# Kernel optimization log

Hardware: AMD Instinct MI355X
Metric: run time of the kernel (lower is better)

Reference implementation:

```python
import jax, jax.numpy as jnp
import numpy as np

D, Z, A, H, E = 1024, 256, 32, 512, 1024  # deterministic, state, action, stochastic(hidden), embedding
MIN_STD = 0.1


def _linear_params(key, out_dim, in_dim, scale=0.02):
    kw, kb = jax.random.split(key)
    W = jax.random.normal(kw, (out_dim, in_dim), jnp.float32) * scale
    b = jax.random.normal(kb, (out_dim,), jnp.float32) * scale
    return W, b


def setup_inputs() -> dict:
    key = jax.random.key(0)
    ks = jax.random.split(key, 16)
    T, B = 64, 512
    inp = {
        "prev_state": jax.random.normal(ks[0], (B, Z), jnp.float32),
        "prev_belief": jax.random.normal(ks[1], (B, D), jnp.float32),
        "actions": jax.random.normal(ks[2], (T, B, A), jnp.float32),
        "observations": jax.random.normal(ks[3], (T, B, E), jnp.float32),
        "nonterminals": jnp.ones((T, B, 1), jnp.float32),
        "noise_belief": jax.random.normal(ks[4], (T, B, D), jnp.float32),
        "noise_prior": jax.random.normal(ks[5], (T, B, Z), jnp.float32),
        "noise_post": jax.random.normal(ks[6], (T, B, Z), jnp.float32),
    }
    inp["W_sa"], inp["b_sa"] = _linear_params(ks[7], D, Z + A)      # fc_embed_state_action
    inp["W_ih"], inp["b_ih"] = _linear_params(ks[8], 3 * D, D)       # GRUCell input weights
    inp["W_hh"], inp["b_hh"] = _linear_params(ks[9], 3 * D, D)       # GRUCell hidden weights
    inp["W_eb"], inp["b_eb"] = _linear_params(ks[10], H, D)          # fc_embed_belief
    inp["W_bq"], inp["b_bq"] = _linear_params(ks[11], 2 * D, H)      # fc_belief_posterior
    inp["W_ebp"], inp["b_ebp"] = _linear_params(ks[12], H, D)        # fc_embed_belief_prior
    inp["W_sp"], inp["b_sp"] = _linear_params(ks[13], 2 * Z, H)      # fc_state_prior
    inp["W_ebq"], inp["b_ebq"] = _linear_params(ks[14], H, D + E)    # fc_embed_belief_posterior
    inp["W_sq"], inp["b_sq"] = _linear_params(ks[15], 2 * Z, H)      # fc_state_posterior
    return inp


def _gru_cell(x, h, W_ih, b_ih, W_hh, b_hh):
    gi = x @ W_ih.T + b_ih
    gh = h @ W_hh.T + b_hh
    i_r, i_z, i_n = jnp.split(gi, 3, axis=-1)
    h_r, h_z, h_n = jnp.split(gh, 3, axis=-1)
    r = jax.nn.sigmoid(i_r + h_r)
    z = jax.nn.sigmoid(i_z + h_z)
    n = jnp.tanh(i_n + r * h_n)
    return (1.0 - z) * n + z * h


def rssm_scan(prev_state, prev_belief, actions, observations, nonterminals,
              noise_belief, noise_prior, noise_post,
              W_sa, b_sa, W_ih, b_ih, W_hh, b_hh, W_eb, b_eb, W_bq, b_bq,
              W_ebp, b_ebp, W_sp, b_sp, W_ebq, b_ebq, W_sq, b_sq):
    # t==0 skips the nonterminal mask; shift nonterminals by one and prepend ones
    nt_seq = jnp.concatenate([jnp.ones_like(nonterminals[:1]), nonterminals[:-1]], axis=0)

    def step(carry, xs):
        belief, state = carry
        a_t, o_t, nt_t, nb_t, np_t, nq_t = xs
        s = state * nt_t
        deter_hidden = jax.nn.relu(jnp.concatenate([s, a_t], axis=1) @ W_sa.T + b_sa)
        rnn_out = _gru_cell(deter_hidden, belief, W_ih, b_ih, W_hh, b_hh)
        # stochastic belief
        sh = jax.nn.relu(rnn_out @ W_eb.T + b_eb)
        b_mean, b_raw_std = jnp.split(sh @ W_bq.T + b_bq, 2, axis=1)
        b_std = jax.nn.softplus(b_raw_std) + MIN_STD
        new_belief = b_mean + b_std * nb_t
        # prior
        sh_p = jax.nn.relu(new_belief @ W_ebp.T + b_ebp)
        p_mean, p_raw_std = jnp.split(sh_p @ W_sp.T + b_sp, 2, axis=1)
        p_std = jax.nn.softplus(p_raw_std) + MIN_STD
        p_state = p_mean + p_std * np_t
        # posterior (observations provided)
        sh_q = jax.nn.relu(jnp.concatenate([new_belief, o_t], axis=1) @ W_ebq.T + b_ebq)
        q_mean, q_raw_std = jnp.split(sh_q @ W_sq.T + b_sq, 2, axis=1)
        q_std = jax.nn.softplus(q_raw_std) + MIN_STD
        q_state = q_mean + q_std * nq_t
        return (new_belief, q_state), (new_belief, p_state, p_mean, p_std, q_state, q_mean, q_std)

    xs = (actions, observations, nt_seq, noise_belief, noise_prior, noise_post)
    _, ys = jax.lax.scan(step, (prev_belief, prev_state), xs)
    return ys  # each [T, B, dim]


def reference(prev_state, prev_belief, actions, observations, nonterminals,
              noise_belief, noise_prior, noise_post,
              W_sa, b_sa, W_ih, b_ih, W_hh, b_hh, W_eb, b_eb, W_bq, b_bq,
              W_ebp, b_ebp, W_sp, b_sp, W_ebq, b_ebq, W_sq, b_sq):
    return rssm_scan(prev_state, prev_belief, actions, observations, nonterminals,
                     noise_belief, noise_prior, noise_post,
                     W_sa, b_sa, W_ih, b_ih, W_hh, b_hh, W_eb, b_eb, W_bq, b_bq,
                     W_ebp, b_ebp, W_sp, b_sp, W_ebq, b_ebq, W_sq, b_sq)
```

## Files before the change

### kernel.cpp

```cpp
#include <hip/hip_runtime.h>
#include <hip/hip_bf16.h>
#include <math.h>


using bf16 = __hip_bfloat16;
using short8 = __attribute__((ext_vector_type(8))) short;
using f32x4 = __attribute__((ext_vector_type(4))) float;

__device__ __forceinline__ float sp_f(float x){ return x > 15.f ? x : log1pf(__expf(x)); }
__device__ __forceinline__ float sg_f(float x){ return 1.f/(1.f+__expf(-x)); }
__device__ __forceinline__ float b2f(bf16 x){ return __bfloat162float(x); }
__device__ __forceinline__ bf16  f2b(float x){ return __float2bfloat16(x); }

__device__ __forceinline__ int aoff(int r, int c, int ldk) {
  return r*ldk + (c & ~63) + ((((c>>3)&7) ^ (r&7))<<3) + (c&7);
}

template<int KC, typename AR>
__device__ __forceinline__ void gemm4(f32x4 acc[4], const bf16* __restrict__ wpf,
                                      int lane, AR aread) {
#pragma unroll 2
  for (int kc = 0; kc < KC; ++kc) {
    short8 a = aread(kc*32);
#pragma unroll
    for (int q = 0; q < 4; ++q) {
      short8 b = *(const short8*)(wpf + ((size_t)q*KC + kc)*512 + lane*8);
      asm("v_mfma_f32_16x16x32_bf16 %0, %1, %2, %0" : "+v"(acc[q]) : "v"(a), "v"(b));
    }
  }
}

struct SP {
  const float *prev_state, *prev_belief, *actions, *nonterm, *nb, *nq;
  const bf16 *w_sa, *w_gru, *w_eb, *w_bq, *w_ebq, *w_sq;
  const float *bg, *b_sa, *b_eb, *b_bq, *b_sq;
  const bf16 *obs_c;
  float *o_bel, *o_qst, *o_qm, *o_qsd;
};

__global__ __launch_bounds__(512) void scan_k(SP p) {
  __shared__ bf16 sB[16*1024];
  __shared__ bf16 sD[16*1024];
  __shared__ bf16 sR[16*1024];
  const int tid = threadIdx.x, l = tid & 63, w2 = tid >> 6;
  const int fl = l & 15, fg = l >> 4;
  const int rbase = blockIdx.x * 16;

  if (tid < 256) {
    const int r = tid >> 4;
    const int c0 = (tid & 15) * 64;
    const float* src = p.prev_belief + (size_t)(rbase + r)*1024 + c0;
#pragma unroll
    for (int s = 0; s < 8; ++s) {
      float4 a = *(const float4*)(src + s*8);
      float4 b = *(const float4*)(src + s*8 + 4);
      bf16 t8[8] __attribute__((aligned(16)));
      t8[0]=f2b(a.x); t8[1]=f2b(a.y); t8[2]=f2b(a.z); t8[3]=f2b(a.w);
      t8[4]=f2b(b.x); t8[5]=f2b(b.y); t8[6]=f2b(b.z); t8[7]=f2b(b.w);
      *(short8*)(sB + aoff(r, c0 + s*8, 1024)) = *(const short8*)t8;
    }
    const int c1 = (tid & 15) * 16;
    const float* sq2 = p.prev_state + (size_t)(rbase + r)*256 + c1;
#pragma unroll
    for (int s = 0; s < 2; ++s) {
      float4 a = *(const float4*)(sq2 + s*8);
      float4 b = *(const float4*)(sq2 + s*8 + 4);
      bf16 t8[8] __attribute__((aligned(16)));
      t8[0]=f2b(a.x); t8[1]=f2b(a.y); t8[2]=f2b(a.z); t8[3]=f2b(a.w);
      t8[4]=f2b(b.x); t8[5]=f2b(b.y); t8[6]=f2b(b.z); t8[7]=f2b(b.w);
      *(short8*)(sR + aoff(r, c1 + s*8, 320)) = *(const short8*)t8;
    }
  } else if (tid < 320) {
    const int r = (tid-256) >> 2, c0 = 288 + ((tid-256)&3)*8;
    bf16 z8[8] __attribute__((aligned(16))) = {};
    *(short8*)(sR + aoff(r, c0, 320)) = *(const short8*)z8;
  }
  __syncthreads();

#pragma unroll 1
  for (int t = 0; t < 64; ++t) {
    if (tid < 128) {
      const int r = tid >> 3, cc = (tid & 7) * 4;
      float4 a = *(const float4*)(p.actions + (size_t)(t*512 + rbase + r)*32 + cc);
      sR[aoff(r, 256+cc,   320)] = f2b(a.x);
      sR[aoff(r, 256+cc+1, 320)] = f2b(a.y);
      sR[aoff(r, 256+cc+2, 320)] = f2b(a.z);
      sR[aoff(r, 256+cc+3, 320)] = f2b(a.w);
    }
    __syncthreads();
    {
      auto aq = [&](int c){ return *(const short8*)(sR + aoff(fl, c + fg*8, 320)); };
#pragma unroll 1
      for (int g = 0; g < 2; ++g) {
        f32x4 acc[4] = {};
        const int f0 = w2*8 + g*4;
        gemm4<10>(acc, p.w_sa + (size_t)f0*10*512, l, aq);
#pragma unroll
        for (int q = 0; q < 4; ++q) {
          const int col = (f0+q)*16 + fl;
          const float bv = p.b_sa[col];
#pragma unroll
          for (int rr = 0; rr < 4; ++rr) {
            float v = acc[q][rr] + bv;
            sD[aoff(fg*4+rr, col, 1024)] = f2b(v > 0.f ? v : 0.f);
          }
        }
      }
    }
    __syncthreads();
    {
#pragma unroll 1
      for (int jj = 0; jj < 8; ++jj) {
        const int jt = w2*8 + jj;
        const bf16* base = p.w_gru + (size_t)jt*32*6*512 + l*8;
        f32x4 ar_ = {}, az_ = {}, ai_ = {}, ah_ = {};
        short8 b0[6], b1[6];
#pragma unroll
        for (int s = 0; s < 6; ++s) b0[s] = *(const short8*)(base + (size_t)s*512);
#pragma unroll 1
        for (int kc = 0; kc < 32; kc += 2) {
#pragma unroll
          for (int s = 0; s < 6; ++s)
            b1[s] = *(const short8*)(base + (size_t)((kc+1)*6 + s)*512);
          short8 ad = *(const short8*)(sD + aoff(fl, kc*32 + fg*8, 1024));
          short8 ab = *(const short8*)(sB + aoff(fl, kc*32 + fg*8, 1024));
          asm("v_mfma_f32_16x16x32_bf16 %0, %1, %2, %0" : "+v"(ar_) : "v"(ad), "v"(b0[0]));
          asm("v_mfma_f32_16x16x32_bf16 %0, %1, %2, %0" : "+v"(az_) : "v"(ad), "v"(b0[1]));
          asm("v_mfma_f32_16x16x32_bf16 %0, %1, %2, %0" : "+v"(ai_) : "v"(ad), "v"(b0[2]));
          asm("v_mfma_f32_16x16x32_bf16 %0, %1, %2, %0" : "+v"(ar_) : "v"(ab), "v"(b0[3]));
          asm("v_mfma_f32_16x16x32_bf16 %0, %1, %2, %0" : "+v"(az_) : "v"(ab), "v"(b0[4]));
          asm("v_mfma_f32_16x16x32_bf16 %0, %1, %2, %0" : "+v"(ah_) : "v"(ab), "v"(b0[5]));
          if (kc + 2 < 32) {
#pragma unroll
            for (int s = 0; s < 6; ++s)
              b0[s] = *(const short8*)(base + (size_t)((kc+2)*6 + s)*512);
          }
          ad = *(const short8*)(sD + aoff(fl, (kc+1)*32 + fg*8, 1024));
          ab = *(const short8*)(sB + aoff(fl, (kc+1)*32 + fg*8, 1024));
          asm("v_mfma_f32_16x16x32_bf16 %0, %1, %2, %0" : "+v"(ar_) : "v"(ad), "v"(b1[0]));
          asm("v_mfma_f32_16x16x32_bf16 %0, %1, %2, %0" : "+v"(az_) : "v"(ad), "v"(b1[1]));
          asm("v_mfma_f32_16x16x32_bf16 %0, %1, %2, %0" : "+v"(ai_) : "v"(ad), "v"(b1[2]));
          asm("v_mfma_f32_16x16x32_bf16 %0, %1, %2, %0" : "+v"(ar_) : "v"(ab), "v"(b1[3]));
          asm("v_mfma_f32_16x16x32_bf16 %0, %1, %2, %0" : "+v"(az_) : "v"(ab), "v"(b1[4]));
          asm("v_mfma_f32_16x16x32_bf16 %0, %1, %2, %0" : "+v"(ah_) : "v"(ab), "v"(b1[5]));
        }
        const int j = jt*16 + fl;
        const float g0 = p.bg[j], g1 = p.bg[1024+j], g2 = p.bg[2048+j], g3 = p.bg[3072+j];
#pragma unroll
        for (int rr = 0; rr < 4; ++rr) {
          const int row = fg*4 + rr;
          const float r_ = sg_f(ar_[rr] + g0);
          const float z_ = sg_f(az_[rr] + g1);
          const float nn = tanhf((ai_[rr] + g2) + r_*(ah_[rr] + g3));
          const float h = b2f(sB[aoff(row, j, 1024)]);
          sR[aoff(row, j, 1024)] = f2b((1.f - z_)*nn + z_*h);
        }
      }
    }
    __syncthreads();
    {
      auto ar = [&](int c){ return *(const short8*)(sR + aoff(fl, c + fg*8, 1024)); };
      f32x4 acc[4] = {};
      const int f0 = w2*4;
      gemm4<32>(acc, p.w_eb + (size_t)f0*32*512, l, ar);
#pragma unroll
      for (int q = 0; q < 4; ++q) {
        const int col = (f0+q)*16 + fl;
        const float bv = p.b_eb[col];
#pragma unroll
        for (int rr = 0; rr < 4; ++rr) {
          float v = acc[q][rr] + bv;
          sD[aoff(fg*4+rr, col, 1024)] = f2b(v > 0.f ? v : 0.f);
        }
      }
    }
    __syncthreads();
    {
      auto as = [&](int c){ return *(const short8*)(sD + aoff(fl, c + fg*8, 1024)); };
      const float* nbt = p.nb + (size_t)(t*512 + rbase)*1024;
      float* obt = p.o_bel + (size_t)(t*512 + rbase)*1024;
#pragma unroll 1
      for (int g = 0; g < 4; ++g) {
        f32x4 acc[4] = {};
        const int f0 = w2*16 + g*4;
        gemm4<16>(acc, p.w_bq + (size_t)f0*16*512, l, as);
#pragma unroll
        for (int jj = 0; jj < 2; ++jj) {
          const int j = (w2*8 + g*2 + jj)*16 + fl;
          const float bm = p.b_bq[j], bs = p.b_bq[1024 + j];
#pragma unroll
          for (int rr = 0; rr < 4; ++rr) {
            const int row = fg*4 + rr;
            const float mean = acc[2*jj][rr] + bm;
            const float sd = sp_f(acc[2*jj+1][rr] + bs) + 0.1f;
            const float bl = mean + sd * nbt[(size_t)row*1024 + j];
            obt[(size_t)row*1024 + j] = bl;
            sB[aoff(row, j, 1024)] = f2b(bl);
          }
        }
      }
    }
    __syncthreads();
    {
      auto ab = [&](int c){ return *(const short8*)(sB + aoff(fl, c + fg*8, 1024)); };
      const bf16* oc = p.obs_c + (size_t)(t*512 + rbase)*512;
      f32x4 acc[4] = {};
      const int f0 = w2*4;
      gemm4<32>(acc, p.w_ebq + (size_t)f0*32*512, l, ab);
#pragma unroll
      for (int q = 0; q < 4; ++q) {
        const int col = (f0+q)*16 + fl;
#pragma unroll
        for (int rr = 0; rr < 4; ++rr) {
          const int row = fg*4 + rr;
          float v = acc[q][rr] + b2f(oc[(size_t)row*512 + col]);
          sD[aoff(row, 512 + col, 1024)] = f2b(v > 0.f ? v : 0.f);
        }
      }
    }
    __syncthreads();
    {
      auto ax = [&](int c){ return *(const short8*)(sD + aoff(fl, 512 + c + fg*8, 1024)); };
      const float* nqt = p.nq + (size_t)(t*512 + rbase)*256;
      float* qm = p.o_qm  + (size_t)(t*512 + rbase)*256;
      float* qs = p.o_qsd + (size_t)(t*512 + rbase)*256;
      float* qt = p.o_qst + (size_t)(t*512 + rbase)*256;
      const float* ntp = p.nonterm + (size_t)t*512 + rbase;
      f32x4 acc[4] = {};
      const int f0 = w2*4;
      gemm4<16>(acc, p.w_sq + (size_t)f0*16*512, l, ax);
#pragma unroll
      for (int jj = 0; jj < 2; ++jj) {
        const int j = (w2*2 + jj)*16 + fl;
        const float bm = p.b_sq[j], bs = p.b_sq[256 + j];
#pragma unroll
        for (int rr = 0; rr < 4; ++rr) {
          const int row = fg*4 + rr;
          const float mean = acc[2*jj][rr] + bm;
          const float sd = sp_f(acc[2*jj+1][rr] + bs) + 0.1f;
          const float q = mean + sd * nqt[(size_t)row*256 + j];
          qm[(size_t)row*256 + j] = mean;
          qs[(size_t)row*256 + j] = sd;
          qt[(size_t)row*256 + j] = q;
          sR[aoff(row, j, 320)] = f2b(q * ntp[row]);
        }
      }
    }
    __syncthreads();
  }
}

__device__ __forceinline__ int lds_off(int row, int slot){ return row*64 + ((slot ^ (row & 7)) << 3); }

__device__ __forceinline__ void glds_tile(const bf16* base, int ld, bf16* buf, int w, int l) {
  const int rsub = l >> 3;
  const int slot = (l & 7) ^ rsub;
  const bf16* src = base + (size_t)(w*32 + rsub)*ld + slot*8;
#pragma unroll
  for (int i = 0; i < 4; ++i)
    __builtin_amdgcn_global_load_lds((const __attribute__((address_space(1))) void*)(src + (size_t)(i*8)*ld),
                                     (__attribute__((address_space(3))) void*)(buf + (w*32 + i*8)*64),
                                     16, 0, 0);
}
__device__ __forceinline__ void glds_tile64(const bf16* base, int ld, bf16* buf, int w, int l) {
  const int rsub = l >> 3;
  const int slot = (l & 7) ^ rsub;
  const bf16* src = base + (size_t)(w*16 + rsub)*ld + slot*8;
#pragma unroll
  for (int i = 0; i < 2; ++i)
    __builtin_amdgcn_global_load_lds((const __attribute__((address_space(1))) void*)(src + (size_t)(i*8)*ld),
                                     (__attribute__((address_space(3))) void*)(buf + (w*16 + i*8)*64),
                                     16, 0, 0);
}

__device__ __forceinline__ void mfma_tiles(f32x4 acc[4][4], const bf16* bA, const bf16* bB,
                                           int wm, int wn, int fl, int fg) {
#pragma unroll
  for (int ks = 0; ks < 2; ++ks) {
    short8 af[4], bfr[4];
#pragma unroll
    for (int i = 0; i < 4; ++i)
      af[i] = *(const short8*)(bA + lds_off(wm*64 + i*16 + fl, ks*4 + fg));
#pragma unroll
    for (int i = 0; i < 4; ++i)
      bfr[i] = *(const short8*)(bB + lds_off(wn*64 + i*16 + fl, ks*4 + fg));
#pragma unroll
    for (int mf = 0; mf < 4; ++mf)
#pragma unroll
      for (int nf = 0; nf < 4; ++nf)
        asm("v_mfma_f32_16x16x32_bf16 %0, %1, %2, %0"
            : "+v"(acc[mf][nf]) : "v"(af[mf]), "v"(bfr[nf]));
  }
}

template<bool RELU>
__device__ void wide_f32_gemm(const float* A, int lda, const bf16* Bw, int ldb, int K,
                              const float* bias, bf16* dst, int ldc) {
  __shared__ bf16 sA0[8192];
  __shared__ bf16 sB0[8192];
  const int tid = threadIdx.x, l = tid & 63, w = tid >> 6;
  const int wm = w >> 1, wn = w & 1, fl = l & 15, fg = l >> 4;
  const int rb = ((int)blockIdx.x >> 2) << 7, nt = blockIdx.x & 3;
  f32x4 acc[4][4] = {};
#pragma unroll 1
  for (int ki = 0; ki < (K >> 6); ++ki) {
    const int k0 = ki << 6;
    glds_tile(Bw + (size_t)(nt*128)*ldb + k0, ldb, sB0, w, l);
#pragma unroll
    for (int i = 0; i < 4; ++i) {
      const int sid = tid + (i << 8);
      const int row = sid >> 3, s = sid & 7;
      const float* src = A + (size_t)(rb + row)*lda + k0 + s*8;
      float4 a = ((const float4*)src)[0], b = ((const float4*)src)[1];
      bf16 t8[8] __attribute__((aligned(16)));
      t8[0]=f2b(a.x); t8[1]=f2b(a.y); t8[2]=f2b(a.z); t8[3]=f2b(a.w);
      t8[4]=f2b(b.x); t8[5]=f2b(b.y); t8[6]=f2b(b.z); t8[7]=f2b(b.w);
      *(short8*)(sA0 + lds_off(row, s)) = *(const short8*)t8;
    }
    asm volatile("s_waitcnt vmcnt(0) lgkmcnt(0)" ::: "memory");
    __builtin_amdgcn_s_barrier();
    mfma_tiles(acc, sA0, sB0, wm, wn, fl, fg);
    __builtin_amdgcn_s_barrier();
  }
#pragma unroll
  for (int mf = 0; mf < 4; ++mf)
#pragma unroll
    for (int nf = 0; nf < 4; ++nf) {
      const int col = nt*128 + wn*64 + nf*16 + fl;
      const float bv = bias[col];
#pragma unroll
      for (int r = 0; r < 4; ++r) {
        const int row = rb + wm*64 + mf*16 + fg*4 + r;
        float v = acc[mf][nf][r] + bv;
        if (RELU) v = v > 0.f ? v : 0.f;
        dst[(size_t)row*ldc + col] = f2b(v);
      }
    }
}

__global__ __launch_bounds__(256) void obsc_k(const float* obs, const bf16* webqh,
                                              const float* b_ebq, bf16* obs_c) {
  wide_f32_gemm<false>(obs, 1024, webqh, 1024, 1024, b_ebq, obs_c, 512);
}
__global__ __launch_bounds__(256) void shp_k(const float* bel, const bf16* webp,
                                             const float* b_ebp, bf16* shp) {
  wide_f32_gemm<true>(bel, 1024, webp, 1024, 1024, b_ebp, shp, 512);
}

__global__ __launch_bounds__(256) void phead_k(const bf16* shp, const bf16* wsp,
    const float* b_sp, const float* np, float* o_pm, float* o_psd, float* o_pst) {
  __shared__ bf16 stA[64*64];
  __shared__ bf16 stB[128*64];
  __shared__ float stash[64*256];
  const int tid = threadIdx.x, l = tid & 63, w = tid >> 6;
  const int wm = w >> 1, wn = w & 1, fl = l & 15, fg = l >> 4;
  const int R0 = blockIdx.x * 64;
#pragma unroll 1
  for (int nt = 0; nt < 4; ++nt) {
    f32x4 acc[2][4] = {};
#pragma unroll 1
    for (int kc = 0; kc < 8; ++kc) {
      glds_tile64(shp + (size_t)R0*512 + kc*64, 512, stA, w, l);
      glds_tile(wsp + (size_t)(nt*128)*512 + kc*64, 512, stB, w, l);
      asm volatile("s_waitcnt vmcnt(0)" ::: "memory");
      __builtin_amdgcn_s_barrier();
#pragma unroll
      for (int ks = 0; ks < 2; ++ks) {
        short8 af[2], bfr[4];
#pragma unroll
        for (int mf = 0; mf < 2; ++mf)
          af[mf] = *(const short8*)(stA + lds_off(wm*32 + mf*16 + fl, ks*4 + fg));
#pragma unroll
        for (int nf = 0; nf < 4; ++nf)
          bfr[nf] = *(const short8*)(stB + lds_off(wn*64 + nf*16 + fl, ks*4 + fg));
#pragma unroll
        for (int mf = 0; mf < 2; ++mf)
#pragma unroll
          for (int nf = 0; nf < 4; ++nf)
            asm("v_mfma_f32_16x16x32_bf16 %0, %1, %2, %0"
                : "+v"(acc[mf][nf]) : "v"(af[mf]), "v"(bfr[nf]));
      }
      __builtin_amdgcn_s_barrier();
    }
#pragma unroll
    for (int mf = 0; mf < 2; ++mf)
#pragma unroll
      for (int gg = 0; gg < 2; ++gg) {
        const int j = nt*64 + (wn*2 + gg)*16 + fl;
        const float bm = b_sp[j], bs = b_sp[256 + j];
#pragma unroll
        for (int rr = 0; rr < 4; ++rr) {
          const int rl = wm*32 + mf*16 + fg*4 + rr;
          const float mean = acc[mf][2*gg][rr] + bm;
          const float sd = sp_f(acc[mf][2*gg+1][rr] + bs) + 0.1f;
          o_pm [(size_t)(R0+rl)*256 + j] = mean;
          o_psd[(size_t)(R0+rl)*256 + j] = sd;
          stash[rl*256 + j] = mean + sd * np[(size_t)(R0+rl)*256 + j];
        }
      }
  }
  __syncthreads();
#pragma unroll 1
  for (int i = tid; i < 4096; i += 256) {
    const int r = i >> 6, c4 = (i & 63) << 2;
    *(float4*)(o_pst + (size_t)(R0+r)*256 + c4) = *(const float4*)(stash + r*256 + c4);
  }
}

__global__ __launch_bounds__(256) void k_pack(const float* __restrict__ src, bf16* __restrict__ dst,
    int NF, int KC, int Ksrc, int ldsrc, int rowoff, int pair, int halfN) {
  const int idx = blockIdx.x*256 + threadIdx.x;
  if (idx >= NF*KC*64) return;
  const int lane = idx & 63, kc = (idx >> 6) % KC, fi = idx / (64*KC);
  int col;
  if (pair) { const int jt = fi >> 1, pp = fi & 1; col = pp*halfN + jt*16 + (lane & 15); }
  else col = fi*16 + (lane & 15);
  const int kb = kc*32 + (lane >> 4)*8;
  bf16 t8[8] __attribute__((aligned(16)));
#pragma unroll
  for (int e = 0; e < 8; ++e) {
    const int k = kb + e;
    t8[e] = f2b(k < Ksrc ? src[(size_t)col*ldsrc + rowoff + k] : 0.f);
  }
  *(short8*)(dst + (size_t)idx*8) = *(const short8*)t8;
}

__global__ __launch_bounds__(256) void k_gru_pack6(const float* __restrict__ Wih,
    const float* __restrict__ Whh, bf16* __restrict__ dst) {
  const int idx = blockIdx.x*256 + threadIdx.x;
  if (idx >= 786432) return;
  const int lane = idx & 63;
  const int rest = idx >> 6;
  const int slot = rest % 6;
  const int tkc  = rest / 6;
  const int kc = tkc & 31, jt = tkc >> 5;
  const int j = jt*16 + (lane & 15);
  const int kb = kc*32 + (lane >> 4)*8;
  const float* src;
  if (slot == 0)      src = Wih + (size_t)j*1024;
  else if (slot == 1) src = Wih + (size_t)(1024+j)*1024;
  else if (slot == 2) src = Wih + (size_t)(2048+j)*1024;
  else if (slot == 3) src = Whh + (size_t)j*1024;
  else if (slot == 4) src = Whh + (size_t)(1024+j)*1024;
  else                src = Whh + (size_t)(2048+j)*1024;
  bf16 t8[8] __attribute__((aligned(16)));
#pragma unroll
  for (int e = 0; e < 8; ++e) t8[e] = f2b(src[kb + e]);
  *(short8*)(dst + (size_t)idx*8) = *(const short8*)t8;
}

__global__ __launch_bounds__(256) void k_cvt8(const float* __restrict__ s, bf16* __restrict__ d, int n8) {
  const int i = blockIdx.x*256 + threadIdx.x;
  if (i >= n8) return;
  float4 a = ((const float4*)s)[i*2], b = ((const float4*)s)[i*2+1];
  bf16 t8[8] __attribute__((aligned(16)));
  t8[0]=f2b(a.x); t8[1]=f2b(a.y); t8[2]=f2b(a.z); t8[3]=f2b(a.w);
  t8[4]=f2b(b.x); t8[5]=f2b(b.y); t8[6]=f2b(b.z); t8[7]=f2b(b.w);
  ((short8*)d)[i] = *(const short8*)t8;
}
__global__ __launch_bounds__(256) void k_cvthalf(const float* __restrict__ s, bf16* __restrict__ d) {
  const int i = blockIdx.x*256 + threadIdx.x;
  if (i >= 65536) return;
  const int r = i >> 7, c8 = (i & 127)*8;
  const float* sp2 = s + (size_t)r*2048 + 1024 + c8;
  float4 a = ((const float4*)sp2)[0], b = ((const float4*)sp2)[1];
  bf16 t8[8] __attribute__((aligned(16)));
  t8[0]=f2b(a.x); t8[1]=f2b(a.y); t8[2]=f2b(a.z); t8[3]=f2b(a.w);
  t8[4]=f2b(b.x); t8[5]=f2b(b.y); t8[6]=f2b(b.z); t8[7]=f2b(b.w);
  *(short8*)(d + (size_t)i*8) = *(const short8*)t8;
}
__global__ __launch_bounds__(256) void k_pair(const float* __restrict__ src, bf16* __restrict__ dst,
                                              int halfN, int n) {
  const int idx = blockIdx.x*256 + threadIdx.x;
  if (idx >= n) return;
  const int rp = idx >> 7;
  const int c4 = (idx & 127) << 2;
  const int nt = rp >> 7, id = rp & 127;
  const int pb = (id >> 5) & 3, comp = (id >> 4) & 1, fl2 = id & 15;
  const int j = nt*64 + pb*16 + fl2;
  const int srow = comp*halfN + j;
  float4 v = *(const float4*)(src + (size_t)srow*512 + c4);
  bf16 t4[4] __attribute__((aligned(8)));
  t4[0]=f2b(v.x); t4[1]=f2b(v.y); t4[2]=f2b(v.z); t4[3]=f2b(v.w);
  *(uint2*)(dst + (size_t)rp*512 + c4) = *(const uint2*)t4;
}
__global__ __launch_bounds__(256) void k_bg(const float* b_ih, const float* b_hh, float* bg) {
  const int i = blockIdx.x*256 + threadIdx.x;
  if (i >= 4096) return;
  const int g = i >> 10, j = i & 1023;
  float v;
  if (g == 0) v = b_ih[j] + b_hh[j];
  else if (g == 1) v = b_ih[1024+j] + b_hh[1024+j];
  else if (g == 2) v = b_ih[2048+j];
  else v = b_hh[2048+j];
  bg[i] = v;
}

extern "C" void kernel_launch(void* const* d_in, const int* in_sizes, int n_in,
                              void* d_out, int out_size, void* d_ws, size_t ws_size,
                              hipStream_t stream) {
  const float* prev_state   = (const float*)d_in[0];
  const float* prev_belief  = (const float*)d_in[1];
  const float* actions      = (const float*)d_in[2];
  const float* observations = (const float*)d_in[3];
  const float* nonterm      = (const float*)d_in[4];
  const float* noise_belief = (const float*)d_in[5];
  const float* noise_prior  = (const float*)d_in[6];
  const float* noise_post   = (const float*)d_in[7];
  const float* W_sa  = (const float*)d_in[8];  const float* b_sa  = (const float*)d_in[9];
  const float* W_ih  = (const float*)d_in[10]; const float* b_ih  = (const float*)d_in[11];
  const float* W_hh  = (const float*)d_in[12]; const float* b_hh  = (const float*)d_in[13];
  const float* W_eb  = (const float*)d_in[14]; const float* b_eb  = (const float*)d_in[15];
  const float* W_bq  = (const float*)d_in[16]; const float* b_bq  = (const float*)d_in[17];
  const float* W_ebp = (const float*)d_in[18]; const float* b_ebp = (const float*)d_in[19];
  const float* W_sp  = (const float*)d_in[20]; const float* b_sp  = (const float*)d_in[21];
  const float* W_ebq = (const float*)d_in[22]; const float* b_ebq = (const float*)d_in[23];
  const float* W_sq  = (const float*)d_in[24]; const float* b_sq  = (const float*)d_in[25];

  float* out = (float*)d_out;
  char* ws = (char*)d_ws;

  float* bg   = (float*)ws;
  bf16* wb    = (bf16*)(ws + 16384);
  bf16* w_sa  = wb;
  bf16* w_gru = wb + 327680;
  bf16* w_eb  = wb + 6619136;
  bf16* w_bq  = wb + 7143424;
  bf16* w_ebq = wb + 8192000;
  bf16* w_sq  = wb + 8716288;
  bf16* w_ebqh= wb + 8978432;
  bf16* w_ebp = wb + 9502720;
  bf16* w_sp  = wb + 10027008;

  float* o_bel = out;
  float* o_pst = out + 33554432;
  float* o_pm  = out + 41943040;
  float* o_psd = out + 50331648;
  float* o_qst = out + 58720256;
  float* o_qm  = out + 67108864;
  float* o_qsd = out + 75497472;
  bf16* obs_c = (bf16*)o_pm;
  bf16* shp   = (bf16*)o_pst;

  k_bg       <<<16,   256, 0, stream>>>(b_ih, b_hh, bg);
  k_pack     <<<160,  256, 0, stream>>>(W_sa, w_sa, 64, 10, 288, 288, 0, 0, 0);
  k_gru_pack6<<<3072, 256, 0, stream>>>(W_ih, W_hh, w_gru);
  k_pack     <<<256,  256, 0, stream>>>(W_eb, w_eb, 32, 32, 1024, 1024, 0, 0, 0);
  k_pack     <<<512,  256, 0, stream>>>(W_bq, w_bq, 128, 16, 512, 512, 0, 1, 1024);
  k_pack     <<<256,  256, 0, stream>>>(W_ebq, w_ebq, 32, 32, 1024, 2048, 0, 0, 0);
  k_pack     <<<128,  256, 0, stream>>>(W_sq, w_sq, 32, 16, 512, 512, 0, 1, 256);
  k_cvthalf  <<<256,  256, 0, stream>>>(W_ebq, w_ebqh);
  k_cvt8     <<<256,  256, 0, stream>>>(W_ebp, w_ebp, 65536);
  k_pair     <<<256,  256, 0, stream>>>(W_sp, w_sp, 256, 65536);

  obsc_k<<<1024, 256, 0, stream>>>(observations, w_ebqh, b_ebq, obs_c);

  SP p;
  p.prev_state = prev_state; p.prev_belief = prev_belief; p.actions = actions;
  p.nonterm = nonterm; p.nb = noise_belief; p.nq = noise_post;
  p.w_sa = w_sa; p.w_gru = w_gru; p.w_eb = w_eb; p.w_bq = w_bq; p.w_ebq = w_ebq; p.w_sq = w_sq;
  p.bg = bg; p.b_sa = b_sa; p.b_eb = b_eb; p.b_bq = b_bq; p.b_sq = b_sq;
  p.obs_c = obs_c;
  p.o_bel = o_bel; p.o_qst = o_qst; p.o_qm = o_qm; p.o_qsd = o_qsd;
  scan_k<<<32, 512, 0, stream>>>(p);

  shp_k  <<<1024, 256, 0, stream>>>(o_bel, w_ebp, b_ebp, shp);
  phead_k<<<512,  256, 0, stream>>>(shp, w_sp, b_sp, noise_prior, o_pm, o_psd, o_pst);
}
```

Measured before the change: 12.01 ms.

## Double scan kernel block to 1024 threads and software-pipeline weight loads

New measurement: 12.27 ms. 1.02x slower.

```diff
diff --git a/kernel.cpp b/kernel.cpp
--- a/kernel.cpp
+++ b/kernel.cpp
@@ -16,17 +16,31 @@
   return r*ldk + (c & ~63) + ((((c>>3)&7) ^ (r&7))<<3) + (c&7);
 }
 
-template<int KC, typename AR>
-__device__ __forceinline__ void gemm4(f32x4 acc[4], const bf16* __restrict__ wpf,
+template<int NF, int KC, typename AR>
+__device__ __forceinline__ void gemmN(f32x4 acc[NF], const bf16* __restrict__ wpf,
                                       int lane, AR aread) {
-#pragma unroll 2
-  for (int kc = 0; kc < KC; ++kc) {
+  short8 b0[NF], b1[NF];
+#pragma unroll
+  for (int s = 0; s < NF; ++s)
+    b0[s] = *(const short8*)(wpf + ((size_t)s*KC)*512 + lane*8);
+#pragma unroll 1
+  for (int kc = 0; kc < KC; kc += 2) {
+#pragma unroll
+    for (int s = 0; s < NF; ++s)
+      b1[s] = *(const short8*)(wpf + ((size_t)s*KC + kc + 1)*512 + lane*8);
     short8 a = aread(kc*32);
 #pragma unroll
-    for (int q = 0; q < 4; ++q) {
-      short8 b = *(const short8*)(wpf + ((size_t)q*KC + kc)*512 + lane*8);
-      asm("v_mfma_f32_16x16x32_bf16 %0, %1, %2, %0" : "+v"(acc[q]) : "v"(a), "v"(b));
-    }
+    for (int s = 0; s < NF; ++s)
+      asm("v_mfma_f32_16x16x32_bf16 %0, %1, %2, %0" : "+v"(acc[s]) : "v"(a), "v"(b0[s]));
+    if (kc + 2 < KC) {
+#pragma unroll
+      for (int s = 0; s < NF; ++s)
+        b0[s] = *(const short8*)(wpf + ((size_t)s*KC + kc + 2)*512 + lane*8);
+    }
+    a = aread((kc+1)*32);
+#pragma unroll
+    for (int s = 0; s < NF; ++s)
+      asm("v_mfma_f32_16x16x32_bf16 %0, %1, %2, %0" : "+v"(acc[s]) : "v"(a), "v"(b1[s]));
   }
 }
 
@@ -38,11 +52,11 @@
   float *o_bel, *o_qst, *o_qm, *o_qsd;
 };
 
-__global__ __launch_bounds__(512) void scan_k(SP p) {
+__global__ __launch_bounds__(1024) void scan_k(SP p) {
   __shared__ bf16 sB[16*1024];
   __shared__ bf16 sD[16*1024];
   __shared__ bf16 sR[16*1024];
-  const int tid = threadIdx.x, l = tid & 63, w2 = tid >> 6;
+  const int tid = threadIdx.x, l = tid & 63, w3 = tid >> 6;
   const int fl = l & 15, fg = l >> 4;
   const int rbase = blockIdx.x * 16;
 
@@ -90,28 +104,25 @@
     __syncthreads();
     {
       auto aq = [&](int c){ return *(const short8*)(sR + aoff(fl, c + fg*8, 320)); };
-#pragma unroll 1
-      for (int g = 0; g < 2; ++g) {
-        f32x4 acc[4] = {};
-        const int f0 = w2*8 + g*4;
-        gemm4<10>(acc, p.w_sa + (size_t)f0*10*512, l, aq);
-#pragma unroll
-        for (int q = 0; q < 4; ++q) {
-          const int col = (f0+q)*16 + fl;
-          const float bv = p.b_sa[col];
-#pragma unroll
-          for (int rr = 0; rr < 4; ++rr) {
-            float v = acc[q][rr] + bv;
-            sD[aoff(fg*4+rr, col, 1024)] = f2b(v > 0.f ? v : 0.f);
-          }
+      f32x4 acc[4] = {};
+      const int f0 = w3*4;
+      gemmN<4,10>(acc, p.w_sa + (size_t)f0*10*512, l, aq);
+#pragma unroll
+      for (int q = 0; q < 4; ++q) {
+        const int col = (f0+q)*16 + fl;
+        const float bv = p.b_sa[col];
+#pragma unroll
+        for (int rr = 0; rr < 4; ++rr) {
+          float v = acc[q][rr] + bv;
+          sD[aoff(fg*4+rr, col, 1024)] = f2b(v > 0.f ? v : 0.f);
         }
       }
     }
     __syncthreads();
     {
 #pragma unroll 1
-      for (int jj = 0; jj < 8; ++jj) {
-        const int jt = w2*8 + jj;
+      for (int jj = 0; jj < 4; ++jj) {
+        const int jt = w3*4 + jj;
         const bf16* base = p.w_gru + (size_t)jt*32*6*512 + l*8;
         f32x4 ar_ = {}, az_ = {}, ai_ = {}, ah_ = {};
         short8 b0[6], b1[6];
@@ -160,11 +171,11 @@
     __syncthreads();
     {
       auto ar = [&](int c){ return *(const short8*)(sR + aoff(fl, c + fg*8, 1024)); };
-      f32x4 acc[4] = {};
-      const int f0 = w2*4;
-      gemm4<32>(acc, p.w_eb + (size_t)f0*32*512, l, ar);
-#pragma unroll
-      for (int q = 0; q < 4; ++q) {
+      f32x4 acc[2] = {};
+      const int f0 = w3*2;
+      gemmN<2,32>(acc, p.w_eb + (size_t)f0*32*512, l, ar);
+#pragma unroll
+      for (int q = 0; q < 2; ++q) {
         const int col = (f0+q)*16 + fl;
         const float bv = p.b_eb[col];
 #pragma unroll
@@ -180,13 +191,13 @@
       const float* nbt = p.nb + (size_t)(t*512 + rbase)*1024;
       float* obt = p.o_bel + (size_t)(t*512 + rbase)*1024;
 #pragma unroll 1
-      for (int g = 0; g < 4; ++g) {
+      for (int g = 0; g < 2; ++g) {
         f32x4 acc[4] = {};
-        const int f0 = w2*16 + g*4;
-        gemm4<16>(acc, p.w_bq + (size_t)f0*16*512, l, as);
+        const int f0 = w3*8 + g*4;
+        gemmN<4,16>(acc, p.w_bq + (size_t)f0*16*512, l, as);
 #pragma unroll
         for (int jj = 0; jj < 2; ++jj) {
-          const int j = (w2*8 + g*2 + jj)*16 + fl;
+          const int j = (w3*4 + g*2 + jj)*16 + fl;
           const float bm = p.b_bq[j], bs = p.b_bq[1024 + j];
 #pragma unroll
           for (int rr = 0; rr < 4; ++rr) {
@@ -204,11 +215,11 @@
     {
       auto ab = [&](int c){ return *(const short8*)(sB + aoff(fl, c + fg*8, 1024)); };
       const bf16* oc = p.obs_c + (size_t)(t*512 + rbase)*512;
-      f32x4 acc[4] = {};
-      const int f0 = w2*4;
-      gemm4<32>(acc, p.w_ebq + (size_t)f0*32*512, l, ab);
-#pragma unroll
-      for (int q = 0; q < 4; ++q) {
+      f32x4 acc[2] = {};
+      const int f0 = w3*2;
+      gemmN<2,32>(acc, p.w_ebq + (size_t)f0*32*512, l, ab);
+#pragma unroll
+      for (int q = 0; q < 2; ++q) {
         const int col = (f0+q)*16 + fl;
 #pragma unroll
         for (int rr = 0; rr < 4; ++rr) {
@@ -226,24 +237,21 @@
       float* qs = p.o_qsd + (size_t)(t*512 + rbase)*256;
       float* qt = p.o_qst + (size_t)(t*512 + rbase)*256;
       const float* ntp = p.nonterm + (size_t)t*512 + rbase;
-      f32x4 acc[4] = {};
-      const int f0 = w2*4;
-      gemm4<16>(acc, p.w_sq + (size_t)f0*16*512, l, ax);
-#pragma unroll
-      for (int jj = 0; jj < 2; ++jj) {
-        const int j = (w2*2 + jj)*16 + fl;
-        const float bm = p.b_sq[j], bs = p.b_sq[256 + j];
-#pragma unroll
-        for (int rr = 0; rr < 4; ++rr) {
-          const int row = fg*4 + rr;
-          const float mean = acc[2*jj][rr] + bm;
-          const float sd = sp_f(acc[2*jj+1][rr] + bs) + 0.1f;
-          const float q = mean + sd * nqt[(size_t)row*256 + j];
-          qm[(size_t)row*256 + j] = mean;
-          qs[(size_t)row*256 + j] = sd;
-          qt[(size_t)row*256 + j] = q;
-          sR[aoff(row, j, 320)] = f2b(q * ntp[row]);
-        }
+      f32x4 acc[2] = {};
+      const int f0 = w3*2;
+      gemmN<2,16>(acc, p.w_sq + (size_t)f0*16*512, l, ax);
+      const int j = w3*16 + fl;
+      const float bm = p.b_sq[j], bs = p.b_sq[256 + j];
+#pragma unroll
+      for (int rr = 0; rr < 4; ++rr) {
+        const int row = fg*4 + rr;
+        const float mean = acc[0][rr] + bm;
+        const float sd = sp_f(acc[1][rr] + bs) + 0.1f;
+        const float q = mean + sd * nqt[(size_t)row*256 + j];
+        qm[(size_t)row*256 + j] = mean;
+        qs[(size_t)row*256 + j] = sd;
+        qt[(size_t)row*256 + j] = q;
+        sR[aoff(row, j, 320)] = f2b(q * ntp[row]);
       }
     }
     __syncthreads();
@@ -562,7 +570,7 @@
   p.bg = bg; p.b_sa = b_sa; p.b_eb = b_eb; p.b_bq = b_bq; p.b_sq = b_sq;
   p.obs_c = obs_c;
   p.o_bel = o_bel; p.o_qst = o_qst; p.o_qm = o_qm; p.o_qsd = o_qsd;
-  scan_k<<<32, 512, 0, stream>>>(p);
+  scan_k<<<32, 1024, 0, stream>>>(p);
 
   shp_k  <<<1024, 256, 0, stream>>>(o_bel, w_ebp, b_ebp, shp);
   phead_k<<<512,  256, 0, stream>>>(shp, w_sp, b_sp, noise_prior, o_pm, o_psd, o_pst);
```
